# Kernel tuning notes

Measured on AMD Instinct MI355X. Metric: run time of the kernel, lower is better.

The kernel has to match this reference:

```python
import jax, jax.numpy as jnp
import numpy as np

TOP_K = 8
EPS_NORM = 1e-12  # torch F.normalize eps
EPS_ENT = 1e-9

B, N, D = 8, 1024, 512


def setup_inputs() -> dict:
    key = jax.random.key(0)
    ks = jax.random.split(key, 16)
    inp = {}
    for i in range(8):
        inp[f"band{i}"] = jax.random.normal(ks[i], (B, N, D), dtype=jnp.float32)
    s = 1.0 / np.sqrt(D)
    inp["qW"] = jax.random.normal(ks[8], (8, D, D), dtype=jnp.float32) * s
    inp["qb"] = jax.random.normal(ks[9], (8, D), dtype=jnp.float32) * s
    inp["kW"] = jax.random.normal(ks[10], (8, D, D), dtype=jnp.float32) * s
    inp["kb"] = jax.random.normal(ks[11], (8, D), dtype=jnp.float32) * s
    inp["vW"] = jax.random.normal(ks[12], (8, D, D), dtype=jnp.float32) * s
    inp["vb"] = jax.random.normal(ks[13], (8, D), dtype=jnp.float32) * s
    return inp


def _l2norm(x):
    n = jnp.linalg.norm(x, axis=-1, keepdims=True)
    return x / jnp.maximum(n, EPS_NORM)


def _cross_attend(q_band, kv_band, q_idx, k_idx, qW, qb, kW, kb, vW, vb):
    # Linear: x @ W.T + b
    Q = jnp.einsum('bnd,ed->bne', q_band, qW[q_idx]) + qb[q_idx]
    K = jnp.einsum('bnd,ed->bne', kv_band, kW[k_idx]) + kb[k_idx]
    V = jnp.einsum('bnd,ed->bne', kv_band, vW[k_idx]) + vb[k_idx]
    Qn, Kn = _l2norm(Q), _l2norm(K)
    scores = jnp.einsum('bqd,bkd->bqk', Qn, Kn)  # cosine sims, [B,Nq,Nk]
    b, nq, nk = scores.shape
    _, idx = jax.lax.top_k(scores, TOP_K)  # [B,Nq,k]
    mask = jnp.zeros(scores.shape, dtype=bool).at[
        jnp.arange(b)[:, None, None], jnp.arange(nq)[None, :, None], idx
    ].set(True)
    scores = jnp.where(mask, scores, -jnp.inf)
    attn = jax.nn.softmax(scores, axis=-1)
    entropy = -(attn * jnp.log(attn + EPS_ENT)).sum(-1).mean(1)  # [B]
    out = jnp.einsum('bqk,bkd->bqd', attn, V)
    return out, entropy


def reference(band0, band1, band2, band3, band4, band5, band6, band7,
              qW, qb, kW, kb, vW, vb):
    bands = [band0, band1, band2, band3, band4, band5, band6, band7]
    outputs = list(bands)
    entropies = []

    def ca(qi, ki):
        return _cross_attend(bands[qi], bands[ki], qi, ki, qW, qb, kW, kb, vW, vb)

    # complementary pairs
    for lo, hi in [(0, 6), (1, 5), (2, 4)]:
        o, e = ca(hi, lo)
        outputs[hi] = outputs[hi] + o
        entropies.append(e)
        o, e = ca(lo, hi)
        outputs[lo] = outputs[lo] + o
        entropies.append(e)
    # bridge band 3 -> all spectral
    for i in [0, 1, 2, 4, 5, 6]:
        o, e = ca(i, 3)
        outputs[i] = outputs[i] + 0.5 * o
        entropies.append(e)
    # temporal band 7 -> all
    for i in range(7):
        o, e = ca(i, 7)
        outputs[i] = outputs[i] + 0.5 * o
        entropies.append(e)

    return jnp.stack(outputs, 0), jnp.stack(entropies, 0)  # [8,B,N,D], [19,B]
```

## Files before the change

kernel.cpp:

```cpp
#include <hip/hip_runtime.h>
#include <math.h>

#define B_ 8
#define N_ 1024
#define D_ 512
#define BAND_ELEMS (B_ * N_ * D_)
#define OUT_MAIN (8L * BAND_ELEMS)
#define NCALLS 19

struct Ptrs8 { const float* p[8]; };
struct CallTab { int qi[NCALLS]; int ki[NCALLS]; };
struct MergeTab { int ncalls[8]; int calls[8][3]; int kis[NCALLS]; float wts[NCALLS]; };

typedef __attribute__((ext_vector_type(8))) short bf16x8;
typedef __attribute__((ext_vector_type(8))) ushort ushort8;
typedef __attribute__((ext_vector_type(4))) float f32x4;

__device__ __forceinline__ ushort f2bf_rne(float x) {
  uint u = __float_as_uint(x);
  return (ushort)((u + 0x7fffu + ((u >> 16) & 1u)) >> 16);
}
__device__ __forceinline__ float bf2f(ushort h) {
  return __uint_as_float(((uint)h) << 16);
}

#define GLOAD16(gsrc, ldst)                                                   \
  __builtin_amdgcn_global_load_lds(                                          \
      (const __attribute__((address_space(1))) void*)(gsrc),                 \
      (__attribute__((address_space(3))) void*)(ldst), 16, 0, 0)
#define GLOAD4(gsrc, ldst)                                                    \
  __builtin_amdgcn_global_load_lds(                                          \
      (const __attribute__((address_space(1))) void*)(gsrc),                 \
      (__attribute__((address_space(3))) void*)(ldst), 4, 0, 0)

__device__ __forceinline__ void bitonic64_desc(float& v, int& i) {
  const int lane = threadIdx.x & 63;
#pragma unroll
  for (int k = 2; k <= 64; k <<= 1) {
#pragma unroll
    for (int j = 64; j > 0; j >>= 1) {
      if (j > (k >> 1)) continue;
      float ov = __shfl_xor(v, j);
      int oi = __shfl_xor(i, j);
      const bool up = (lane & k) == 0;
      const bool lower = (lane & j) == 0;
      const bool mineFirst = (v > ov) || (v == ov && i < oi);
      const bool keep = (up == lower) ? mineFirst : !mineFirst;
      if (!keep) { v = ov; i = oi; }
    }
  }
}

#define BM 128
#define BN 128
#define BK 16
#define LDP 132

__device__ __forceinline__ int bgran(int g) {
  return (g & ~7) | ((g + (g >> 3)) & 7);
}

__device__ __forceinline__ void gemm_core(const float* __restrict__ A,
                                          const float* __restrict__ Bm,
                                          int m0, int n0, int K,
                                          float (&acc)[8][8]) {
  __shared__ float As[BK * LDP];
  __shared__ float Bs[BK * LDP];

  const int t = threadIdx.x;
  const int tx = t & 15, ty = t >> 4;
  const int rs = t >> 2;
  const int cs = t & 3;

  float4 pa[2], pb[2];
#pragma unroll
  for (int it = 0; it < 2; ++it) {
    pa[it] = *(const float4*)(A + (long)(m0 + rs + 64 * it) * K + cs * 4);
    pb[it] = *(const float4*)(Bm + (long)(n0 + rs + 64 * it) * K + cs * 4);
  }

  for (int k0 = 0; k0 < K; k0 += BK) {
    __syncthreads();
    {
      const int sa = ((cs & 1) << 2);
      const int base = cs * 4 * LDP;
#pragma unroll
      for (int it = 0; it < 2; ++it) {
        const int r = rs + 64 * it;
        const int ra = r ^ sa;
        As[base + 0 * LDP + ra] = pa[it].x;
        As[base + 1 * LDP + ra] = pa[it].y;
        As[base + 2 * LDP + ra] = pa[it].z;
        As[base + 3 * LDP + ra] = pa[it].w;
        const int rb = bgran(r >> 2) * 4 + (r & 3);
        Bs[base + 0 * LDP + rb] = pb[it].x;
        Bs[base + 1 * LDP + rb] = pb[it].y;
        Bs[base + 2 * LDP + rb] = pb[it].z;
        Bs[base + 3 * LDP + rb] = pb[it].w;
      }
    }
    __syncthreads();

    if (k0 + BK < K) {
#pragma unroll
      for (int it = 0; it < 2; ++it) {
        pa[it] = *(const float4*)(A + (long)(m0 + rs + 64 * it) * K + k0 + BK + cs * 4);
        pb[it] = *(const float4*)(Bm + (long)(n0 + rs + 64 * it) * K + k0 + BK + cs * 4);
      }
    }

#pragma unroll
    for (int kk = 0; kk < BK; ++kk) {
      const int c1 = (kk >> 2) & 1;
      float a[8], b[8];
      {
        float4 u = *(const float4*)&As[kk * LDP + ty * 8 + c1 * 4];
        float4 v = *(const float4*)&As[kk * LDP + ty * 8 + 4 - c1 * 4];
        a[0] = u.x; a[1] = u.y; a[2] = u.z; a[3] = u.w;
        a[4] = v.x; a[5] = v.y; a[6] = v.z; a[7] = v.w;
        float4 p = *(const float4*)&Bs[kk * LDP + bgran(2 * tx) * 4];
        float4 q = *(const float4*)&Bs[kk * LDP + bgran(2 * tx + 1) * 4];
        b[0] = p.x; b[1] = p.y; b[2] = p.z; b[3] = p.w;
        b[4] = q.x; b[5] = q.y; b[6] = q.z; b[7] = q.w;
      }
#pragma unroll
      for (int i = 0; i < 8; ++i)
#pragma unroll
        for (int j = 0; j < 8; ++j) acc[i][j] = fmaf(a[i], b[j], acc[i][j]);
    }
  }
}

__device__ __forceinline__ void proj_epilogue(float* __restrict__ dst,
                                              const float* __restrict__ bvec,
                                              int m0, int n0, float (&acc)[8][8]) {
  const int t = threadIdx.x;
  const int tx = t & 15, ty = t >> 4;
#pragma unroll
  for (int i = 0; i < 8; ++i) {
    float* crow = dst + (long)(m0 + ty * 8 + i) * D_ + n0 + tx * 8;
    const float* bp = bvec + n0 + tx * 8;
    float4 r0, r1;
    r0.x = acc[i][0] + bp[0]; r0.y = acc[i][1] + bp[1];
    r0.z = acc[i][2] + bp[2]; r0.w = acc[i][3] + bp[3];
    r1.x = acc[i][4] + bp[4]; r1.y = acc[i][5] + bp[5];
    r1.z = acc[i][6] + bp[6]; r1.w = acc[i][7] + bp[7];
    ((float4*)crow)[0] = r0;
    ((float4*)crow)[1] = r1;
  }
}

__global__ __launch_bounds__(256) void gemm_proj_qk(Ptrs8 bands,
                                                    const float* __restrict__ qW,
                                                    const float* __restrict__ kW,
                                                    const float* __restrict__ qb,
                                                    const float* __restrict__ kb,
                                                    float* __restrict__ Qn,
                                                    float* __restrict__ Kn) {
  const int mat = blockIdx.z >> 3, band = blockIdx.z & 7;
  const float* W = (mat == 0) ? qW : kW;
  const float* bvec = (mat == 0) ? qb : kb;
  float* dst = ((mat == 0) ? Qn : Kn) + (long)band * BAND_ELEMS;
  W += (long)band * D_ * D_;
  bvec += band * D_;

  const int m0 = blockIdx.y * BM, n0 = blockIdx.x * BN;
  float acc[8][8] = {};
  gemm_core(bands.p[band], W, m0, n0, D_, acc);
  proj_epilogue(dst, bvec, m0, n0, acc);
}

__global__ __launch_bounds__(256) void gemm_proj_v_mfma(Ptrs8 bands,
                                                        const float* __restrict__ vW,
                                                        const float* __restrict__ vb,
                                                        float* __restrict__ V) {
  __shared__ ushort plds[4 * 4096];

  const int band = blockIdx.z;
  const uint* Au = (const uint*)bands.p[band];
  const uint* Bu = (const uint*)(vW + (long)band * D_ * D_);
  const float* bvec = vb + band * D_;
  float* dst = V + (long)band * BAND_ELEMS;

  const int t = threadIdx.x;
  const int lane = t & 63;
  const int wave = t >> 6;
  const int wm = wave >> 1, wn = wave & 1;
  const int fr = lane & 15, fh = lane >> 4;
  const int m0 = blockIdx.y * BM, n0 = blockIdx.x * BN;

  f32x4 acc[4][4] = {};

  const int sg_r[2] = {t >> 2, (t + 256) >> 2};
  const int sg_h = t & 3;

  for (int k0 = 0; k0 < D_; k0 += 32) {
    uint4 ga[2][2], gb[2][2];
#pragma unroll
    for (int it = 0; it < 2; ++it) {
      long offA = (long)(m0 + sg_r[it]) * D_ + k0 + sg_h * 8;
      ga[it][0] = *(const uint4*)(Au + offA);
      ga[it][1] = *(const uint4*)(Au + offA + 4);
      long offB = (long)(n0 + sg_r[it]) * D_ + k0 + sg_h * 8;
      gb[it][0] = *(const uint4*)(Bu + offB);
      gb[it][1] = *(const uint4*)(Bu + offB + 4);
    }
    __syncthreads();
#pragma unroll
    for (int op = 0; op < 2; ++op) {
#pragma unroll
      for (int it = 0; it < 2; ++it) {
        uint w[8];
        {
          uint4 w0 = op ? gb[it][0] : ga[it][0];
          uint4 w1 = op ? gb[it][1] : ga[it][1];
          w[0] = w0.x; w[1] = w0.y; w[2] = w0.z; w[3] = w0.w;
          w[4] = w1.x; w[5] = w1.y; w[6] = w1.z; w[7] = w1.w;
        }
        ushort8 vhi, vlo;
#pragma unroll
        for (int e = 0; e < 8; ++e) {
          float x = __uint_as_float(w[e]);
          ushort hb = f2bf_rne(x);
          ushort lb = f2bf_rne(x - bf2f(hb));
          vhi[e] = hb;
          vlo[e] = lb;
        }
        const int ds2 = (sg_h * 128 + sg_r[it]) * 8;
        *(ushort8*)&plds[op * 4096 + ds2] = vhi;
        *(ushort8*)&plds[(2 + op) * 4096 + ds2] = vlo;
      }
    }
    __syncthreads();

    bf16x8 ah[4], bh[4], al[4], bl[4];
#pragma unroll
    for (int i = 0; i < 4; ++i) {
      const int ra = wm * 64 + i * 16 + fr;
      const int rb = wn * 64 + i * 16 + fr;
      ah[i] = *(const bf16x8*)&plds[0 * 4096 + (fh * 128 + ra) * 8];
      bh[i] = *(const bf16x8*)&plds[1 * 4096 + (fh * 128 + rb) * 8];
      al[i] = *(const bf16x8*)&plds[2 * 4096 + (fh * 128 + ra) * 8];
      bl[i] = *(const bf16x8*)&plds[3 * 4096 + (fh * 128 + rb) * 8];
    }

#pragma unroll
    for (int i = 0; i < 4; ++i)
#pragma unroll
      for (int j = 0; j < 4; ++j) {
        acc[i][j] = __builtin_amdgcn_mfma_f32_16x16x32_bf16(ah[i], bh[j], acc[i][j], 0, 0, 0);
        acc[i][j] = __builtin_amdgcn_mfma_f32_16x16x32_bf16(ah[i], bl[j], acc[i][j], 0, 0, 0);
        acc[i][j] = __builtin_amdgcn_mfma_f32_16x16x32_bf16(al[i], bh[j], acc[i][j], 0, 0, 0);
      }
  }

#pragma unroll
  for (int i = 0; i < 4; ++i)
#pragma unroll
    for (int j = 0; j < 4; ++j) {
      const int col = n0 + wn * 64 + j * 16 + fr;
      const float bv = bvec[col];
#pragma unroll
      for (int r = 0; r < 4; ++r) {
        const int row = m0 + wm * 64 + i * 16 + fh * 4 + r;
        dst[(long)row * D_ + col] = acc[i][j][r] + bv;
      }
    }
}

__global__ __launch_bounds__(256) void l2norm_rows(float* __restrict__ X,
                                                   ushort* __restrict__ bf) {
  const long row = (long)blockIdx.x * 4 + (threadIdx.x >> 6);
  const int lane = threadIdx.x & 63;
  float* p = X + row * D_;
  float4 a = ((float4*)p)[lane];
  float4 b = ((float4*)p)[lane + 64];
  float s = a.x * a.x + a.y * a.y + a.z * a.z + a.w * a.w +
            b.x * b.x + b.y * b.y + b.z * b.z + b.w * b.w;
#pragma unroll
  for (int m = 1; m < 64; m <<= 1) s += __shfl_xor(s, m);
  const float inv = 1.0f / fmaxf(sqrtf(s), 1e-12f);
  a.x *= inv; a.y *= inv; a.z *= inv; a.w *= inv;
  b.x *= inv; b.y *= inv; b.z *= inv; b.w *= inv;
  ((float4*)p)[lane] = a;
  ((float4*)p)[lane + 64] = b;
  ushort4 w0, w1;
  w0.x = f2bf_rne(a.x); w0.y = f2bf_rne(a.y); w0.z = f2bf_rne(a.z); w0.w = f2bf_rne(a.w);
  w1.x = f2bf_rne(b.x); w1.y = f2bf_rne(b.y); w1.z = f2bf_rne(b.z); w1.w = f2bf_rne(b.w);
  *(ushort4*)(bf + row * D_ + lane * 4) = w0;
  *(ushort4*)(bf + row * D_ + 256 + lane * 4) = w1;
}

#define SBM 128
#define SBN 128

__device__ __forceinline__ int gidx(int row, int oct) {
  return row * 4 + (oct ^ ((row >> 1) & 3));
}

__global__ __launch_bounds__(256) void mfma_extract_bf(const ushort* __restrict__ Qbf,
                                                       const ushort* __restrict__ Kbf,
                                                       float* __restrict__ candv,
                                                       ushort* __restrict__ candi,
                                                       CallTab tab) {
  __shared__ ushort lds[3][2][4096];

  const int z = blockIdx.z;
  const int c = z >> 3, b = z & 7;
  const ushort* A = Qbf + (long)tab.qi[c] * BAND_ELEMS + (long)b * N_ * D_;
  const ushort* Bm = Kbf + (long)tab.ki[c] * BAND_ELEMS + (long)b * N_ * D_;
  const int m0 = blockIdx.y * SBM, n0 = blockIdx.x * SBN;

  const int t = threadIdx.x;
  const int lane = t & 63;
  const int wm = t >> 6;
  const int fr = lane & 15, fh = lane >> 4;

  f32x4 acc[2][8] = {};

  const int srow = lane >> 2;
  const int soct = lane & 3;
  const ushort* sA[2];
  const ushort* sB[2];
  int dof[2];
#pragma unroll
  for (int it = 0; it < 2; ++it) {
    const int row0 = wm * 32 + it * 16;
    const int row = row0 + srow;
    const int oct = soct ^ ((row >> 1) & 3);
    sA[it] = A + (long)(m0 + row) * D_ + oct * 8;
    sB[it] = Bm + (long)(n0 + row) * D_ + oct * 8;
    dof[it] = row0 * 32;
  }

  int gofA[2], gofB[8];
#pragma unroll
  for (int i = 0; i < 2; ++i) gofA[i] = gidx(wm * 32 + i * 16 + fr, fh) * 8;
#pragma unroll
  for (int j = 0; j < 8; ++j) gofB[j] = gidx(j * 16 + fr, fh) * 8;

  ushort* lb = &lds[0][0][0];

#define XSTAGE(buf, m)                                                        \
  do {                                                                        \
    GLOAD16(sA[0] + (m) * 32, lb + ((buf) * 2 + 0) * 4096 + dof[0]);          \
    GLOAD16(sB[0] + (m) * 32, lb + ((buf) * 2 + 1) * 4096 + dof[0]);          \
    GLOAD16(sA[1] + (m) * 32, lb + ((buf) * 2 + 0) * 4096 + dof[1]);          \
    GLOAD16(sB[1] + (m) * 32, lb + ((buf) * 2 + 1) * 4096 + dof[1]);          \
  } while (0)

  XSTAGE(0, 0);
  XSTAGE(1, 1);

#pragma unroll
  for (int kq = 0; kq < 16; ++kq) {
    if (kq < 15) {
      asm volatile("s_waitcnt vmcnt(4)" ::: "memory");
    } else {
      asm volatile("s_waitcnt vmcnt(0)" ::: "memory");
    }
    __builtin_amdgcn_sched_barrier(0);
    __builtin_amdgcn_s_barrier();
    __builtin_amdgcn_sched_barrier(0);

    if (kq + 2 < 16) XSTAGE((kq + 2) % 3, kq + 2);

    const int ph = kq % 3;
    bf16x8 af[2], bfr[8];
#pragma unroll
    for (int i = 0; i < 2; ++i)
      af[i] = *(const bf16x8*)(lb + (ph * 2 + 0) * 4096 + gofA[i]);
#pragma unroll
    for (int j = 0; j < 8; ++j)
      bfr[j] = *(const bf16x8*)(lb + (ph * 2 + 1) * 4096 + gofB[j]);

#pragma unroll
    for (int i = 0; i < 2; ++i)
#pragma unroll
      for (int j = 0; j < 8; ++j)
        acc[i][j] = __builtin_amdgcn_mfma_f32_16x16x32_bf16(af[i], bfr[j], acc[i][j], 0, 0, 0);
  }
#undef XSTAGE

#pragma unroll
  for (int i = 0; i < 2; ++i)
#pragma unroll
    for (int rr = 0; rr < 4; ++rr) {
      const int R = b * N_ + m0 + wm * 32 + i * 16 + fh * 4 + rr;
      const long base = (((long)c * 8192 + R) * 8 + blockIdx.x) * 8;
#pragma unroll
      for (int it = 0; it < 8; ++it) {
        float lv = acc[i][0][rr]; int lj = 0;
#pragma unroll
        for (int j = 1; j < 8; ++j)
          if (acc[i][j][rr] > lv) { lv = acc[i][j][rr]; lj = j; }
        int li = lj * 16 + fr;
#pragma unroll
        for (int m = 1; m < 16; m <<= 1) {
          float ov = __shfl_xor(lv, m);
          int oi = __shfl_xor(li, m);
          if (ov > lv || (ov == lv && oi < li)) { lv = ov; li = oi; }
        }
        if (fr == it) { candv[base + it] = lv; candi[base + it] = (ushort)(n0 + li); }
        if (fr == (li & 15)) {
#pragma unroll
          for (int j = 0; j < 8; ++j)
            if (j == (li >> 4)) acc[i][j][rr] = -INFINITY;
        }
      }
    }
}

#define RRBLOCKS (NCALLS * 8192 / 4)

__global__ __launch_bounds__(256) void rerank_exact(const float* __restrict__ Qn,
                                                    const float* __restrict__ Kn,
                                                    const float* __restrict__ candv,
                                                    const ushort* __restrict__ candi,
                                                    float* __restrict__ fp,
                                                    int* __restrict__ fi,
                                                    float* __restrict__ out,
                                                    CallTab tab) {
  __shared__ float sbuf[4][2][1088];

  const int bid = blockIdx.x;
  const int blk = (bid & 7) * (RRBLOCKS / 8) + (bid >> 3);

  const int w = threadIdx.x >> 6, lane = threadIdx.x & 63;
  const long gr = (long)blk * 4 + w;
  const int c = (int)(gr >> 13);
  const int R = (int)(gr & 8191);
  const int b = R >> 10;

  const long cb = gr * 64;
  float cv = candv[cb + lane];
  int ci = (int)candi[cb + lane];

  bitonic64_desc(cv, ci);
  const int mycand = lane & 15;
  const int eidx = __shfl(ci, mycand);

  const float* qrow = Qn + (long)tab.qi[c] * BAND_ELEMS + (long)R * D_;
  const float* ksrc0 = Kn + (long)tab.ki[c] * BAND_ELEMS +
                       ((long)(b << 10) + eidx) * D_ + ((lane >> 4) << 2);

#define STAGE(bb, ch)                                                         \
  do {                                                                        \
    float* base_ = &sbuf[w][bb][0];                                           \
    GLOAD16(ksrc0 + (ch) * 64 + 0,  base_ + 0);                               \
    GLOAD16(ksrc0 + (ch) * 64 + 16, base_ + 256);                             \
    GLOAD16(ksrc0 + (ch) * 64 + 32, base_ + 512);                             \
    GLOAD16(ksrc0 + (ch) * 64 + 48, base_ + 768);                             \
    GLOAD4(qrow + (ch) * 64 + lane, base_ + 1024);                            \
  } while (0)

  float acc = 0.f;
  STAGE(0, 0);
#pragma unroll
  for (int ch = 0; ch < 8; ++ch) {
    if (ch < 7) {
      STAGE((ch + 1) & 1, ch + 1);
      asm volatile("s_waitcnt vmcnt(5)" ::: "memory");
    } else {
      asm volatile("s_waitcnt vmcnt(0)" ::: "memory");
    }
    const float* kb2 = &sbuf[w][ch & 1][0];
    const float* qb2 = &sbuf[w][ch & 1][1024];
#pragma unroll
    for (int kq = 0; kq < 16; ++kq) {
      float4 kv = *(const float4*)(kb2 + kq * 64 + mycand * 4);
      float4 qv = *(const float4*)(qb2 + kq * 4);
      acc = fmaf(qv.x, kv.x, acc);
      acc = fmaf(qv.y, kv.y, acc);
      acc = fmaf(qv.z, kv.z, acc);
      acc = fmaf(qv.w, kv.w, acc);
    }
  }
#undef STAGE

  float ev = acc; int ei = eidx;
  bitonic64_desc(ev, ei);
  float sv[8]; int si[8];
#pragma unroll
  for (int j = 0; j < 8; ++j) {
    sv[j] = __shfl(ev, 4 * j);
    si[j] = __shfl(ei, 4 * j);
  }

  float p[8], sum = 0.f;
#pragma unroll
  for (int j = 0; j < 8; ++j) { p[j] = expf(sv[j] - sv[0]); sum += p[j]; }
  const float isum = 1.0f / sum;
  float H = 0.f;
#pragma unroll
  for (int j = 0; j < 8; ++j) { p[j] *= isum; H -= p[j] * logf(p[j] + 1e-9f); }

  if (lane == 0) {
    atomicAdd(out + OUT_MAIN + (long)c * B_ + b, H * (1.0f / (float)N_));
#pragma unroll
    for (int j = 0; j < 8; ++j) { fp[gr * 8 + j] = p[j]; fi[gr * 8 + j] = si[j]; }
  }
}

__global__ __launch_bounds__(256) void merge_pv(Ptrs8 bands,
                                                const float* __restrict__ fp,
                                                const int* __restrict__ fi,
                                                const float* __restrict__ V,
                                                float* __restrict__ out,
                                                MergeTab mt) {
  const int bb = blockIdx.y;
  const int w = threadIdx.x >> 6, lane = threadIdx.x & 63;
  const long R = (long)blockIdx.x * 4 + w;
  const int b = (int)(R >> 10);

  float4 o0 = {0, 0, 0, 0}, o1 = {0, 0, 0, 0};
  const int nc = mt.ncalls[bb];
  for (int s = 0; s < nc; ++s) {
    const int c = mt.calls[bb][s];
    const float wt = mt.wts[c];
    const int ki = mt.kis[c];
    const long fb = ((long)c * 8192 + R) * 8;
    float4 p0 = *(const float4*)(fp + fb);
    float4 p1 = *(const float4*)(fp + fb + 4);
    int4 i0 = *(const int4*)(fi + fb);
    int4 i1 = *(const int4*)(fi + fb + 4);
    float pj[8] = {p0.x, p0.y, p0.z, p0.w, p1.x, p1.y, p1.z, p1.w};
    int ij[8] = {i0.x, i0.y, i0.z, i0.w, i1.x, i1.y, i1.z, i1.w};
#pragma unroll
    for (int j = 0; j < 8; ++j) {
      const float pw = pj[j] * wt;
      const float4* vr = (const float4*)(V + (long)ki * BAND_ELEMS +
                                         ((long)(b << 10) + ij[j]) * D_);
      float4 x0 = vr[lane * 2], x1 = vr[lane * 2 + 1];
      o0.x += pw * x0.x; o0.y += pw * x0.y; o0.z += pw * x0.z; o0.w += pw * x0.w;
      o1.x += pw * x1.x; o1.y += pw * x1.y; o1.z += pw * x1.z; o1.w += pw * x1.w;
    }
  }

  const float4* src = (const float4*)(bands.p[bb] + R * D_);
  float4 s0 = src[lane * 2], s1 = src[lane * 2 + 1];
  s0.x += o0.x; s0.y += o0.y; s0.z += o0.z; s0.w += o0.w;
  s1.x += o1.x; s1.y += o1.y; s1.z += o1.z; s1.w += o1.w;
  float4* dst = (float4*)(out + (long)bb * BAND_ELEMS + R * D_);
  dst[lane * 2] = s0;
  dst[lane * 2 + 1] = s1;
}

__global__ void init_eps(float* __restrict__ out) {
  if (threadIdx.x < NCALLS * B_) out[OUT_MAIN + threadIdx.x] = 0.f;
}

extern "C" void kernel_launch(void* const* d_in, const int* in_sizes, int n_in,
                              void* d_out, int out_size, void* d_ws, size_t ws_size,
                              hipStream_t stream) {
  Ptrs8 bands;
  for (int i = 0; i < 8; ++i) bands.p[i] = (const float*)d_in[i];
  const float* qW = (const float*)d_in[8];
  const float* qb = (const float*)d_in[9];
  const float* kW = (const float*)d_in[10];
  const float* kb = (const float*)d_in[11];
  const float* vW = (const float*)d_in[12];
  const float* vb = (const float*)d_in[13];
  float* out = (float*)d_out;
  float* ws = (float*)d_ws;

  float* Qn = ws;
  float* Kn = ws + (long)8 * BAND_ELEMS;
  float* V = ws + (long)16 * BAND_ELEMS;
  ushort* bfbuf = (ushort*)V;
  float* candv = ws + (long)24 * BAND_ELEMS;
  ushort* candi = (ushort*)(candv + (long)NCALLS * 8192 * 64);
  float* fp = (float*)(candi + (long)NCALLS * 8192 * 64);
  int* fi = (int*)(fp + (long)NCALLS * 8192 * 8);

  static const int calls[NCALLS][2] = {
      {6, 0}, {0, 6}, {5, 1}, {1, 5}, {4, 2}, {2, 4},
      {0, 3}, {1, 3}, {2, 3}, {4, 3}, {5, 3}, {6, 3},
      {0, 7}, {1, 7}, {2, 7}, {3, 7}, {4, 7}, {5, 7}, {6, 7}};

  CallTab tab;
  MergeTab mt;
  for (int i = 0; i < 8; ++i) mt.ncalls[i] = 0;
  for (int c = 0; c < NCALLS; ++c) {
    tab.qi[c] = calls[c][0];
    tab.ki[c] = calls[c][1];
    mt.kis[c] = calls[c][1];
    mt.wts[c] = (c < 6) ? 1.0f : 0.5f;
    int q = calls[c][0];
    mt.calls[q][mt.ncalls[q]++] = c;
  }

  hipLaunchKernelGGL(init_eps, dim3(1), dim3(256), 0, stream, out);

  dim3 gqk(D_ / BN, (B_ * N_) / BM, 16);
  hipLaunchKernelGGL(gemm_proj_qk, gqk, dim3(256), 0, stream,
                     bands, qW, kW, qb, kb, Qn, Kn);

  hipLaunchKernelGGL(l2norm_rows, dim3(2 * 8 * B_ * N_ / 4), dim3(256), 0, stream,
                     Qn, bfbuf);

  dim3 gs(N_ / SBN, N_ / SBM, NCALLS * 8);
  hipLaunchKernelGGL(mfma_extract_bf, gs, dim3(256), 0, stream,
                     bfbuf, bfbuf + (long)8 * BAND_ELEMS, candv, candi, tab);

  dim3 gv(D_ / BN, (B_ * N_) / BM, 8);
  hipLaunchKernelGGL(gemm_proj_v_mfma, gv, dim3(256), 0, stream, bands, vW, vb, V);

  hipLaunchKernelGGL(rerank_exact, dim3(RRBLOCKS), dim3(256), 0, stream,
                     Qn, Kn, candv, candi, fp, fi, out, tab);

  hipLaunchKernelGGL(merge_pv, dim3(B_ * N_ / 4, 8), dim3(256), 0, stream,
                     bands, fp, fi, V, out, mt);
}
```

Before: 2.808 ms.

## Double the M-tile of the score-extraction GEMM to 256 rows with 512 threads

The cosine-score MFMA kernel now uses 256-row Q tiles per block with 8 waves instead of 128 rows with 4 waves, so each loaded K tile is shared by twice as many query rows. The LDS layout is restructured so each stage holds an 8192-element A region and a 4096-element B region. Each thread now issues three global-to-LDS loads per stage instead of four, and the wait count drops from vmcnt(4) to vmcnt(3) to match. This cuts K-tile global traffic and block count, at the cost of larger LDS use per block and fewer blocks in flight.

```diff
diff --git a/kernel.cpp b/kernel.cpp
--- a/kernel.cpp
+++ b/kernel.cpp
@@ -291,19 +291,21 @@
   *(ushort4*)(bf + row * D_ + 256 + lane * 4) = w1;
 }
 
-#define SBM 128
+#define SBM 256
 #define SBN 128
+#define APL 8192
+#define BPL 4096
 
 __device__ __forceinline__ int gidx(int row, int oct) {
   return row * 4 + (oct ^ ((row >> 1) & 3));
 }
 
-__global__ __launch_bounds__(256) void mfma_extract_bf(const ushort* __restrict__ Qbf,
+__global__ __launch_bounds__(512) void mfma_extract_bf(const ushort* __restrict__ Qbf,
                                                        const ushort* __restrict__ Kbf,
                                                        float* __restrict__ candv,
                                                        ushort* __restrict__ candi,
                                                        CallTab tab) {
-  __shared__ ushort lds[3][2][4096];
+  __shared__ ushort lds[3][APL + BPL];
 
   const int z = blockIdx.z;
   const int c = z >> 3, b = z & 7;
@@ -321,32 +323,37 @@
   const int srow = lane >> 2;
   const int soct = lane & 3;
   const ushort* sA[2];
-  const ushort* sB[2];
-  int dof[2];
+  const ushort* sB0;
+  int dofA[2], dofB;
 #pragma unroll
   for (int it = 0; it < 2; ++it) {
     const int row0 = wm * 32 + it * 16;
     const int row = row0 + srow;
     const int oct = soct ^ ((row >> 1) & 3);
     sA[it] = A + (long)(m0 + row) * D_ + oct * 8;
-    sB[it] = Bm + (long)(n0 + row) * D_ + oct * 8;
-    dof[it] = row0 * 32;
+    dofA[it] = row0 * 32;
+  }
+  {
+    const int row0 = wm * 16;
+    const int row = row0 + srow;
+    const int oct = soct ^ ((row >> 1) & 3);
+    sB0 = Bm + (long)(n0 + row) * D_ + oct * 8;
+    dofB = APL + row0 * 32;
   }
 
   int gofA[2], gofB[8];
 #pragma unroll
   for (int i = 0; i < 2; ++i) gofA[i] = gidx(wm * 32 + i * 16 + fr, fh) * 8;
 #pragma unroll
-  for (int j = 0; j < 8; ++j) gofB[j] = gidx(j * 16 + fr, fh) * 8;
-
-  ushort* lb = &lds[0][0][0];
+  for (int j = 0; j < 8; ++j) gofB[j] = APL + gidx(j * 16 + fr, fh) * 8;
+
+  ushort* lb = &lds[0][0];
 
 #define XSTAGE(buf, m)                                                        \
   do {                                                                        \
-    GLOAD16(sA[0] + (m) * 32, lb + ((buf) * 2 + 0) * 4096 + dof[0]);          \
-    GLOAD16(sB[0] + (m) * 32, lb + ((buf) * 2 + 1) * 4096 + dof[0]);          \
-    GLOAD16(sA[1] + (m) * 32, lb + ((buf) * 2 + 0) * 4096 + dof[1]);          \
-    GLOAD16(sB[1] + (m) * 32, lb + ((buf) * 2 + 1) * 4096 + dof[1]);          \
+    GLOAD16(sA[0] + (m) * 32, lb + (buf) * (APL + BPL) + dofA[0]);            \
+    GLOAD16(sA[1] + (m) * 32, lb + (buf) * (APL + BPL) + dofA[1]);            \
+    GLOAD16(sB0 + (m) * 32, lb + (buf) * (APL + BPL) + dofB);                 \
   } while (0)
 
   XSTAGE(0, 0);
@@ -355,7 +362,7 @@
 #pragma unroll
   for (int kq = 0; kq < 16; ++kq) {
     if (kq < 15) {
-      asm volatile("s_waitcnt vmcnt(4)" ::: "memory");
+      asm volatile("s_waitcnt vmcnt(3)" ::: "memory");
     } else {
       asm volatile("s_waitcnt vmcnt(0)" ::: "memory");
     }
@@ -366,13 +373,14 @@
     if (kq + 2 < 16) XSTAGE((kq + 2) % 3, kq + 2);
 
     const int ph = kq % 3;
+    const int pb = ph * (APL + BPL);
     bf16x8 af[2], bfr[8];
 #pragma unroll
     for (int i = 0; i < 2; ++i)
-      af[i] = *(const bf16x8*)(lb + (ph * 2 + 0) * 4096 + gofA[i]);
+      af[i] = *(const bf16x8*)(lb + pb + gofA[i]);
 #pragma unroll
     for (int j = 0; j < 8; ++j)
-      bfr[j] = *(const bf16x8*)(lb + (ph * 2 + 1) * 4096 + gofB[j]);
+      bfr[j] = *(const bf16x8*)(lb + pb + gofB[j]);
 
 #pragma unroll
     for (int i = 0; i < 2; ++i)
@@ -600,7 +608,7 @@
                      Qn, bfbuf);
 
   dim3 gs(N_ / SBN, N_ / SBM, NCALLS * 8);
-  hipLaunchKernelGGL(mfma_extract_bf, gs, dim3(256), 0, stream,
+  hipLaunchKernelGGL(mfma_extract_bf, gs, dim3(512), 0, stream,
                      bfbuf, bfbuf + (long)8 * BAND_ELEMS, candv, candi, tab);
 
   dim3 gv(D_ / BN, (B_ * N_) / BM, 8);
```

New measurement: 2.765 ms. About the same (-1.5%).
